# Kernel tuning notes

Hardware: AMD Instinct MI355X
Metric: run time of the kernel (lower is better)

## Reference

```python
import jax, jax.numpy as jnp
import numpy as np

N = 50000       # node_num
E_RND = 1600000 # random edges (avg degree 32)
IN = 256        # in_dim
OUT = 128       # out_dim
NB = 10000      # queried nodes batch
SLOPE = 0.1     # leaky_relu slope_ratio


def setup_inputs() -> dict:
    key = jax.random.key(0)
    k = jax.random.split(key, 6)
    feats = jax.random.normal(k[0], (N, IN), dtype=jnp.float32)
    W = jax.random.normal(k[1], (OUT, IN), dtype=jnp.float32) * 0.05
    b = jax.random.normal(k[2], (OUT,), dtype=jnp.float32) * 0.05
    a = jax.random.normal(k[3], (2 * OUT,), dtype=jnp.float32) * 0.05
    rnd = jax.random.randint(k[4], (E_RND, 2), 0, N)
    loops = jnp.stack([jnp.arange(N), jnp.arange(N)], axis=1)  # self-loops, as in torch code
    edges = jnp.concatenate([rnd, loops], axis=0).astype(jnp.int32)  # [E,2] = (dst, src)
    node_idx = jax.random.randint(k[5], (NB,), 0, N).astype(jnp.int32)
    return dict(feats=feats, W=W, b=b, a=a, edges=edges, node_idx=node_idx)


def reference(feats, W, b, a, edges, node_idx):
    n = feats.shape[0]
    emb = feats @ W.T + b                      # [N, OUT]  (out_linear_layer)
    out_dim = emb.shape[1]
    # concat(emb[dst], emb[src]) @ a  ==  (emb @ a1)[dst] + (emb @ a2)[src]
    s_dst = emb @ a[:out_dim]                  # [N]
    s_src = emb @ a[out_dim:]                  # [N]
    dst, src = edges[:, 0], edges[:, 1]
    score = jnp.exp(jax.nn.leaky_relu(s_dst[dst] + s_src[src], negative_slope=SLOPE))  # [E]
    # sparse.mm(matrix, emb) and sparse.mm(matrix, ones) as segment sums over dst
    num = jax.ops.segment_sum(score[:, None] * emb[src], dst, num_segments=n)  # [N, OUT]
    den = jax.ops.segment_sum(score, dst, num_segments=n)                       # [N]
    out = num / den[:, None]
    return out[node_idx]
```

## Files before the change

### kernel.cpp

```cpp
#include <hip/hip_runtime.h>

#define IN_DIM 256
#define OUT_DIM 128
#define SLOPE 0.1f
#define CAP 128

typedef short bf16x8 __attribute__((ext_vector_type(8)));
typedef float f32x4  __attribute__((ext_vector_type(4)));

__device__ __forceinline__ unsigned short f2bf(float f) {
    unsigned u = __builtin_bit_cast(unsigned, f);
    return (unsigned short)((u + 0x7FFFu + ((u >> 16) & 1u)) >> 16);
}

__global__ __launch_bounds__(256) void gemm_mfma_kernel(
    const float* __restrict__ feats, const float* __restrict__ W,
    const float* __restrict__ bias, const float* __restrict__ a,
    unsigned short* __restrict__ emb_bf, float* __restrict__ s_dst,
    float* __restrict__ s_src, int* __restrict__ needed,
    int* __restrict__ cur, int n)
{
    __shared__ __align__(16) unsigned short A_s[64 * 136];
    __shared__ __align__(16) unsigned short W_s[128 * 128];
    __shared__ float sd_l[2][64];
    __shared__ float ss_l[2][64];

    const int t    = threadIdx.x;
    const int lane = t & 63;
    const int wid  = t >> 6;
    const int wr   = wid >> 1;
    const int wc   = wid & 1;
    const int row0 = blockIdx.x * 64;

    if (t < 64) {
        const int ci = row0 + t;
        if (ci < n) { needed[ci] = 0; cur[ci] = 0; }
    }

    const f32x4 z4 = {0.f, 0.f, 0.f, 0.f};
    f32x4 acc[2][4];
    #pragma unroll
    for (int mi = 0; mi < 2; ++mi)
        #pragma unroll
        for (int ni = 0; ni < 4; ++ni) acc[mi][ni] = z4;

    for (int ph = 0; ph < 2; ++ph) {
        const int k0 = ph * 128;
        if (ph) __syncthreads();

        #pragma unroll
        for (int i = 0; i < 4; ++i) {
            const int g = i * 256 + t;
            const int r = g >> 4;
            const int c = g & 15;
            const int gr = row0 + r;
            float4 v0 = make_float4(0.f,0.f,0.f,0.f), v1 = v0;
            if (gr < n) {
                v0 = *(const float4*)&feats[(size_t)gr * IN_DIM + k0 + c * 8];
                v1 = *(const float4*)&feats[(size_t)gr * IN_DIM + k0 + c * 8 + 4];
            }
            bf16x8 pk;
            pk[0]=(short)f2bf(v0.x); pk[1]=(short)f2bf(v0.y);
            pk[2]=(short)f2bf(v0.z); pk[3]=(short)f2bf(v0.w);
            pk[4]=(short)f2bf(v1.x); pk[5]=(short)f2bf(v1.y);
            pk[6]=(short)f2bf(v1.z); pk[7]=(short)f2bf(v1.w);
            const int off = (r * 128 + c * 8) ^ ((r & 7) << 3);
            *(bf16x8*)&A_s[off] = pk;
        }
        #pragma unroll
        for (int i = 0; i < 8; ++i) {
            const int g = i * 256 + t;
            const int r = g >> 4;
            const int c = g & 15;
            const float4 v0 = *(const float4*)&W[(size_t)r * IN_DIM + k0 + c * 8];
            const float4 v1 = *(const float4*)&W[(size_t)r * IN_DIM + k0 + c * 8 + 4];
            bf16x8 pk;
            pk[0]=(short)f2bf(v0.x); pk[1]=(short)f2bf(v0.y);
            pk[2]=(short)f2bf(v0.z); pk[3]=(short)f2bf(v0.w);
            pk[4]=(short)f2bf(v1.x); pk[5]=(short)f2bf(v1.y);
            pk[6]=(short)f2bf(v1.z); pk[7]=(short)f2bf(v1.w);
            const int off = (r * 128 + c * 8) ^ ((r & 7) << 3);
            *(bf16x8*)&W_s[off] = pk;
        }
        __syncthreads();

        #pragma unroll
        for (int ks = 0; ks < 4; ++ks) {
            const int kf = ks * 32 + (lane >> 4) * 8;
            bf16x8 af[2], wf[4];
            #pragma unroll
            for (int mi = 0; mi < 2; ++mi) {
                const int row = wr * 32 + mi * 16 + (lane & 15);
                const int off = (row * 128 + kf) ^ ((row & 7) << 3);
                af[mi] = *(const bf16x8*)&A_s[off];
            }
            #pragma unroll
            for (int ni = 0; ni < 4; ++ni) {
                const int col = wc * 64 + ni * 16 + (lane & 15);
                const int off = (col * 128 + kf) ^ ((col & 7) << 3);
                wf[ni] = *(const bf16x8*)&W_s[off];
            }
            #pragma unroll
            for (int mi = 0; mi < 2; ++mi)
                #pragma unroll
                for (int ni = 0; ni < 4; ++ni)
                    acc[mi][ni] = __builtin_amdgcn_mfma_f32_16x16x32_bf16(
                        af[mi], wf[ni], acc[mi][ni], 0, 0, 0);
        }
    }

    float bcol[4], avd[4], avs[4];
    #pragma unroll
    for (int ni = 0; ni < 4; ++ni) {
        const int col = wc * 64 + ni * 16 + (lane & 15);
        bcol[ni] = bias[col];
        avd[ni]  = a[col];
        avs[ni]  = a[OUT_DIM + col];
    }

    __syncthreads();

    #pragma unroll
    for (int mi = 0; mi < 2; ++mi) {
        #pragma unroll
        for (int j = 0; j < 4; ++j) {
            const int rib = wr * 32 + mi * 16 + (lane >> 4) * 4 + j;
            float pd = 0.f, ps = 0.f;
            #pragma unroll
            for (int ni = 0; ni < 4; ++ni) {
                const float v = acc[mi][ni][j] + bcol[ni];
                A_s[rib * 136 + wc * 64 + ni * 16 + (lane & 15)] = f2bf(v);
                pd = fmaf(v, avd[ni], pd);
                ps = fmaf(v, avs[ni], ps);
            }
            pd += __shfl_xor(pd, 1); ps += __shfl_xor(ps, 1);
            pd += __shfl_xor(pd, 2); ps += __shfl_xor(ps, 2);
            pd += __shfl_xor(pd, 4); ps += __shfl_xor(ps, 4);
            pd += __shfl_xor(pd, 8); ps += __shfl_xor(ps, 8);
            if ((lane & 15) == 0) { sd_l[wc][rib] = pd; ss_l[wc][rib] = ps; }
        }
    }
    __syncthreads();

    #pragma unroll
    for (int i = 0; i < 4; ++i) {
        const int g = i * 256 + t;
        const int r = g >> 4;
        const int c8 = g & 15;
        const int gr = row0 + r;
        if (gr < n) {
            const bf16x8 v = *(const bf16x8*)&A_s[r * 136 + c8 * 8];
            *(bf16x8*)&emb_bf[(size_t)gr * OUT_DIM + c8 * 8] = v;
        }
    }
    if (t < 64) {
        const int row = row0 + t;
        if (row < n) {
            s_dst[row] = sd_l[0][t] + sd_l[1][t];
            s_src[row] = ss_l[0][t] + ss_l[1][t];
        }
    }
}

__global__ void flag_kernel(const int* __restrict__ node_idx,
                            int* __restrict__ needed, int nb)
{
    const int i = blockIdx.x * blockDim.x + threadIdx.x;
    if (i < nb) needed[node_idx[i]] = 1;
}

__global__ __launch_bounds__(256) void scatter_kernel(
    const int* __restrict__ edges, const int* __restrict__ needed,
    int* __restrict__ cur, const float* __restrict__ s_dst,
    const float* __restrict__ s_src, int2* __restrict__ ew, int E)
{
    const int e = blockIdx.x * blockDim.x + threadIdx.x;
    if (e >= E) return;
    const int2 ed = reinterpret_cast<const int2*>(edges)[e];
    if (needed[ed.x]) {
        const float x = s_dst[ed.x] + s_src[ed.y];
        const float w = __expf(x >= 0.f ? x : SLOPE * x);
        const int p = atomicAdd(&cur[ed.x], 1);
        if (p < CAP)
            ew[(size_t)ed.x * CAP + p] = make_int2(ed.y, __float_as_int(w));
    }
}

__global__ __launch_bounds__(256) void agg_out_kernel(
    const int* __restrict__ node_idx, const int* __restrict__ cur,
    const int2* __restrict__ ew, const unsigned short* __restrict__ emb_bf,
    float* __restrict__ out, int nb)
{
    const int w    = (int)((blockIdx.x * blockDim.x + threadIdx.x) >> 6);
    const int lane = threadIdx.x & 63;
    if (w >= nb) return;

    const int dst = node_idx[w];
    int m = cur[dst];
    if (m > CAP) m = CAP;
    const int2* __restrict__ bucket = ew + (size_t)dst * CAP;

    float accx = 0.f, accy = 0.f, den = 0.f;

    for (int base = 0; base < m; base += 64) {
        const int rem = min(64, m - base);
        int   src = 0;
        float wt  = 0.f;
        if (lane < rem) {
            const int2 q = bucket[base + lane];
            src = q.x;
            wt  = __int_as_float(q.y);
        }
        int i = 0;
        for (; i + 4 <= rem; i += 4) {
            const int   s0 = __shfl(src, i),     s1 = __shfl(src, i + 1);
            const int   s2 = __shfl(src, i + 2), s3 = __shfl(src, i + 3);
            const float w0 = __shfl(wt, i),      w1 = __shfl(wt, i + 1);
            const float w2 = __shfl(wt, i + 2),  w3 = __shfl(wt, i + 3);
            const unsigned b0 = *(const unsigned*)&emb_bf[(size_t)s0 * OUT_DIM + 2 * lane];
            const unsigned b1 = *(const unsigned*)&emb_bf[(size_t)s1 * OUT_DIM + 2 * lane];
            const unsigned b2 = *(const unsigned*)&emb_bf[(size_t)s2 * OUT_DIM + 2 * lane];
            const unsigned b3 = *(const unsigned*)&emb_bf[(size_t)s3 * OUT_DIM + 2 * lane];
            den += (w0 + w1) + (w2 + w3);
            accx = fmaf(w0, __int_as_float((int)(b0 << 16)), accx);
            accy = fmaf(w0, __int_as_float((int)(b0 & 0xFFFF0000u)), accy);
            accx = fmaf(w1, __int_as_float((int)(b1 << 16)), accx);
            accy = fmaf(w1, __int_as_float((int)(b1 & 0xFFFF0000u)), accy);
            accx = fmaf(w2, __int_as_float((int)(b2 << 16)), accx);
            accy = fmaf(w2, __int_as_float((int)(b2 & 0xFFFF0000u)), accy);
            accx = fmaf(w3, __int_as_float((int)(b3 << 16)), accx);
            accy = fmaf(w3, __int_as_float((int)(b3 & 0xFFFF0000u)), accy);
        }
        for (; i < rem; ++i) {
            const int   s0 = __shfl(src, i);
            const float w0 = __shfl(wt, i);
            const unsigned b0 = *(const unsigned*)&emb_bf[(size_t)s0 * OUT_DIM + 2 * lane];
            den += w0;
            accx = fmaf(w0, __int_as_float((int)(b0 << 16)), accx);
            accy = fmaf(w0, __int_as_float((int)(b0 & 0xFFFF0000u)), accy);
        }
    }

    const float inv = 1.0f / den;
    float2 o; o.x = accx * inv; o.y = accy * inv;
    *reinterpret_cast<float2*>(&out[(size_t)w * OUT_DIM + 2 * lane]) = o;
}

extern "C" void kernel_launch(void* const* d_in, const int* in_sizes, int n_in,
                              void* d_out, int out_size, void* d_ws, size_t ws_size,
                              hipStream_t stream)
{
    const float* feats    = (const float*)d_in[0];
    const float* W        = (const float*)d_in[1];
    const float* bias     = (const float*)d_in[2];
    const float* a        = (const float*)d_in[3];
    const int*   edges    = (const int*)d_in[4];
    const int*   node_idx = (const int*)d_in[5];
    float*       out      = (float*)d_out;

    const int n  = in_sizes[0] / IN_DIM;
    const int E  = in_sizes[4] / 2;
    const int nb = in_sizes[5];

    char* ws = (char*)d_ws;
    unsigned short* emb_bf = (unsigned short*)ws;
    ws += (size_t)n * OUT_DIM * sizeof(unsigned short);
    float* s_dst = (float*)ws;  ws += (size_t)(n + 4) * sizeof(float);
    float* s_src = (float*)ws;  ws += (size_t)(n + 4) * sizeof(float);
    int*   needed= (int*)ws;    ws += (size_t)(n + 4) * sizeof(int);
    int*   cur   = (int*)ws;    ws += (size_t)(n + 4) * sizeof(int);
    int2*  ew    = (int2*)ws;   ws += (size_t)n * CAP * sizeof(int2);

    gemm_mfma_kernel<<<(n + 63) / 64, 256, 0, stream>>>(
        feats, W, bias, a, emb_bf, s_dst, s_src, needed, cur, n);
    flag_kernel     <<<(nb + 255) / 256, 256, 0, stream>>>(node_idx, needed, nb);
    scatter_kernel  <<<(E + 255) / 256, 256, 0, stream>>>(edges, needed, cur, s_dst, s_src, ew, E);
    agg_out_kernel  <<<(nb + 3) / 4, 256, 0, stream>>>(node_idx, cur, ew, emb_bf, out, nb);
}
```

Before: 65.82 us.

## Load GEMM tiles directly into LDS as fp32 and write embeddings straight to global

The GEMM tile staging now uses global_load_lds to copy fp32 feats and W straight into swizzled shared memory. The bf16 conversion moves to register fragment loads, and the K loop is split into four 64-wide phases. The epilogue writes bf16 embeddings directly to global memory instead of staging them through shared memory, which removes one barrier and a copy pass. In exchange, the W tile and every A fragment are converted again on each fragment read, and the direct 2-byte global stores are less coalesced.

```diff
diff --git a/kernel.cpp b/kernel.cpp
--- a/kernel.cpp
+++ b/kernel.cpp
@@ -11,6 +11,19 @@
 __device__ __forceinline__ unsigned short f2bf(float f) {
     unsigned u = __builtin_bit_cast(unsigned, f);
     return (unsigned short)((u + 0x7FFFu + ((u >> 16) & 1u)) >> 16);
+}
+
+__device__ __forceinline__ void pack8(const float4& v0, const float4& v1, bf16x8& pk) {
+    pk[0]=(short)f2bf(v0.x); pk[1]=(short)f2bf(v0.y);
+    pk[2]=(short)f2bf(v0.z); pk[3]=(short)f2bf(v0.w);
+    pk[4]=(short)f2bf(v1.x); pk[5]=(short)f2bf(v1.y);
+    pk[6]=(short)f2bf(v1.z); pk[7]=(short)f2bf(v1.w);
+}
+
+__device__ __forceinline__ void gld_lds16(const void* g, void* l) {
+    __builtin_amdgcn_global_load_lds(
+        (const __attribute__((address_space(1))) void*)g,
+        (__attribute__((address_space(3))) void*)l, 16, 0, 0);
 }
 
 __global__ __launch_bounds__(256) void gemm_mfma_kernel(
@@ -20,8 +33,8 @@
     float* __restrict__ s_src, int* __restrict__ needed,
     int* __restrict__ cur, int n)
 {
-    __shared__ __align__(16) unsigned short A_s[64 * 136];
-    __shared__ __align__(16) unsigned short W_s[128 * 128];
+    __shared__ __align__(16) float A_s[64 * 64];
+    __shared__ __align__(16) float W_s[128 * 64];
     __shared__ float sd_l[2][64];
     __shared__ float ss_l[2][64];
 
@@ -37,6 +50,9 @@
         if (ci < n) { needed[ci] = 0; cur[ci] = 0; }
     }
 
+    const int rlo4 = lane >> 4;
+    const int b16  = lane & 15;
+
     const f32x4 z4 = {0.f, 0.f, 0.f, 0.f};
     f32x4 acc[2][4];
     #pragma unroll
@@ -44,61 +60,46 @@
         #pragma unroll
         for (int ni = 0; ni < 4; ++ni) acc[mi][ni] = z4;
 
-    for (int ph = 0; ph < 2; ++ph) {
-        const int k0 = ph * 128;
+    for (int ph = 0; ph < 4; ++ph) {
+        const int k0 = ph * 64;
         if (ph) __syncthreads();
 
         #pragma unroll
-        for (int i = 0; i < 4; ++i) {
-            const int g = i * 256 + t;
-            const int r = g >> 4;
-            const int c = g & 15;
-            const int gr = row0 + r;
-            float4 v0 = make_float4(0.f,0.f,0.f,0.f), v1 = v0;
-            if (gr < n) {
-                v0 = *(const float4*)&feats[(size_t)gr * IN_DIM + k0 + c * 8];
-                v1 = *(const float4*)&feats[(size_t)gr * IN_DIM + k0 + c * 8 + 4];
-            }
-            bf16x8 pk;
-            pk[0]=(short)f2bf(v0.x); pk[1]=(short)f2bf(v0.y);
-            pk[2]=(short)f2bf(v0.z); pk[3]=(short)f2bf(v0.w);
-            pk[4]=(short)f2bf(v1.x); pk[5]=(short)f2bf(v1.y);
-            pk[6]=(short)f2bf(v1.z); pk[7]=(short)f2bf(v1.w);
-            const int off = (r * 128 + c * 8) ^ ((r & 7) << 3);
-            *(bf16x8*)&A_s[off] = pk;
-        }
-        #pragma unroll
-        for (int i = 0; i < 8; ++i) {
-            const int g = i * 256 + t;
-            const int r = g >> 4;
-            const int c = g & 15;
-            const float4 v0 = *(const float4*)&W[(size_t)r * IN_DIM + k0 + c * 8];
-            const float4 v1 = *(const float4*)&W[(size_t)r * IN_DIM + k0 + c * 8 + 4];
-            bf16x8 pk;
-            pk[0]=(short)f2bf(v0.x); pk[1]=(short)f2bf(v0.y);
-            pk[2]=(short)f2bf(v0.z); pk[3]=(short)f2bf(v0.w);
-            pk[4]=(short)f2bf(v1.x); pk[5]=(short)f2bf(v1.y);
-            pk[6]=(short)f2bf(v1.z); pk[7]=(short)f2bf(v1.w);
-            const int off = (r * 128 + c * 8) ^ ((r & 7) << 3);
-            *(bf16x8*)&W_s[off] = pk;
+        for (int j = 0; j < 4; ++j) {
+            const int r  = wid * 16 + j * 4 + rlo4;
+            const int gr = min(row0 + r, n - 1);
+            const int ch = b16 ^ ((r & 7) << 1);
+            gld_lds16(feats + (size_t)gr * IN_DIM + k0 + (ch << 2),
+                      &A_s[(wid * 16 + j * 4) * 64]);
+        }
+        #pragma unroll
+        for (int j = 0; j < 8; ++j) {
+            const int c  = wid * 32 + j * 4 + rlo4;
+            const int ch = b16 ^ ((c & 7) << 1);
+            gld_lds16(W + (size_t)c * IN_DIM + k0 + (ch << 2),
+                      &W_s[(wid * 32 + j * 4) * 64]);
         }
         __syncthreads();
 
         #pragma unroll
-        for (int ks = 0; ks < 4; ++ks) {
-            const int kf = ks * 32 + (lane >> 4) * 8;
+        for (int ks = 0; ks < 2; ++ks) {
+            const int c0 = ks * 8 + (lane >> 4) * 2;
             bf16x8 af[2], wf[4];
             #pragma unroll
             for (int mi = 0; mi < 2; ++mi) {
                 const int row = wr * 32 + mi * 16 + (lane & 15);
-                const int off = (row * 128 + kf) ^ ((row & 7) << 3);
-                af[mi] = *(const bf16x8*)&A_s[off];
+                const int cc  = c0 ^ ((row & 7) << 1);
+                const float4 f0 = *(const float4*)&A_s[row * 64 + cc * 4];
+                const float4 f1 = *(const float4*)&A_s[row * 64 + cc * 4 + 4];
+                pack8(f0, f1, af[mi]);
             }
             #pragma unroll
             for (int ni = 0; ni < 4; ++ni) {
                 const int col = wc * 64 + ni * 16 + (lane & 15);
-                const int off = (col * 128 + kf) ^ ((col & 7) << 3);
-                wf[ni] = *(const bf16x8*)&W_s[off];
+                const int cc  = c0 ^ ((col & 7) << 1);
+                const float4 f0 = *(const float4*)&W_s[col * 64 + cc * 4];
+                const float4 f1 = *(const float4*)&W_s[col * 64 + cc * 4 + 4];
+                pack8(f0, f1, wf[ni]);
             }
             #pragma unroll
             for (int mi = 0; mi < 2; ++mi)
@@ -118,20 +119,21 @@
         avs[ni]  = a[OUT_DIM + col];
     }
 
-    __syncthreads();
-
     #pragma unroll
     for (int mi = 0; mi < 2; ++mi) {
         #pragma unroll
         for (int j = 0; j < 4; ++j) {
             const int rib = wr * 32 + mi * 16 + (lane >> 4) * 4 + j;
+            const int row = row0 + rib;
             float pd = 0.f, ps = 0.f;
-            #pragma unroll
-            for (int ni = 0; ni < 4; ++ni) {
-                const float v = acc[mi][ni][j] + bcol[ni];
-                A_s[rib * 136 + wc * 64 + ni * 16 + (lane & 15)] = f2bf(v);
-                pd = fmaf(v, avd[ni], pd);
-                ps = fmaf(v, avs[ni], ps);
+            if (row < n) {
+                #pragma unroll
+                for (int ni = 0; ni < 4; ++ni) {
+                    const float v = acc[mi][ni][j] + bcol[ni];
+                    emb_bf[(size_t)row * OUT_DIM + wc * 64 + ni * 16 + (lane & 15)] = f2bf(v);
+                    pd = fmaf(v, avd[ni], pd);
+                    ps = fmaf(v, avs[ni], ps);
+                }
             }
             pd += __shfl_xor(pd, 1); ps += __shfl_xor(ps, 1);
             pd += __shfl_xor(pd, 2); ps += __shfl_xor(ps, 2);
@@ -141,18 +143,6 @@
         }
     }
     __syncthreads();
-
-    #pragma unroll
-    for (int i = 0; i < 4; ++i) {
-        const int g = i * 256 + t;
-        const int r = g >> 4;
-        const int c8 = g & 15;
-        const int gr = row0 + r;
-        if (gr < n) {
-            const bf16x8 v = *(const bf16x8*)&A_s[r * 136 + c8 * 8];
-            *(bf16x8*)&emb_bf[(size_t)gr * OUT_DIM + c8 * 8] = v;
-        }
-    }
     if (t < 64) {
         const int row = row0 + t;
         if (row < n) {
```

Measured after the change: 66.90 us. Within noise of the previous version (+1.6%).
